# Kernel tuning notes

Measured on AMD Instinct MI355X. Metric: run time of the kernel, lower is better.

Reference implementation:

```python
import jax, jax.numpy as jnp
import numpy as np

B, S, E, H = 4, 2048, 1024, 16
HD = E // H  # head_dim = 64


def setup_inputs() -> dict:
    key = jax.random.key(0)
    k1, k2, k3, k4 = jax.random.split(key, 4)
    x = jax.random.normal(k1, (B, S, E), dtype=jnp.float32)
    # torch Linear stores weight as (out, in); y = x @ W.T
    w_qkv = jax.random.normal(k2, (3 * E, E), dtype=jnp.float32) * (E ** -0.5)
    w_proj = jax.random.normal(k3, (E, E), dtype=jnp.float32) * (E ** -0.5)
    b_proj = jax.random.normal(k4, (E,), dtype=jnp.float32) * 0.01
    return {"x": x, "w_qkv": w_qkv, "w_proj": w_proj, "b_proj": b_proj}


def reference(x, w_qkv, w_proj, b_proj):
    b, s, e = x.shape
    # fused QKV, then per-head interleaved split (matches view(B,S,H,3*hd).chunk)
    qkv = jnp.einsum('bse,fe->bsf', x, w_qkv).reshape(b, s, H, 3 * HD)
    q, k, v = jnp.split(qkv, 3, axis=-1)  # each (b, s, H, HD)
    scale = HD ** -0.5
    scores = jnp.einsum('bqhd,bkhd->bhqk', q, k) * scale
    causal = jnp.tril(jnp.ones((s, s), dtype=bool))
    scores = jnp.where(causal, scores, jnp.float32(-jnp.inf))
    probs = jax.nn.softmax(scores, axis=-1)
    out = jnp.einsum('bhqk,bkhd->bqhd', probs, v).reshape(b, s, e)
    return jnp.einsum('bse,fe->bsf', out, w_proj) + b_proj
```

## Files before the change

kernel.cpp:

```cpp
#include <hip/hip_runtime.h>

#define Bq   4
#define Sq   2048
#define Eq   1024
#define Hq   16
#define HDq  64
#define Mq   (Bq*Sq)
#define N1q  (3*Eq)
#define Kq   Eq

#define NX4  (Mq*Kq/4)
#define NW4  (N1q*Kq/4)
#define NP4  (Eq*Kq/4)

typedef __bf16 bf16x8 __attribute__((ext_vector_type(8)));
typedef __bf16 bf16x4 __attribute__((ext_vector_type(4)));
typedef float  f32x4  __attribute__((ext_vector_type(4)));
typedef float  f32x16 __attribute__((ext_vector_type(16)));

#define GAS __attribute__((address_space(1)))
#define LAS __attribute__((address_space(3)))

__device__ __forceinline__ void gl2lds16(const void* g, void* l) {
  __builtin_amdgcn_global_load_lds((GAS const void*)g, (LAS void*)l, 16, 0, 0);
}

__device__ __forceinline__ unsigned pack2(float a, float b) {
  union { __bf16 h[2]; unsigned u; } x;
  x.h[0] = (__bf16)a; x.h[1] = (__bf16)b; return x.u;
}

__device__ __forceinline__ void perm32swap(unsigned& a, unsigned& b) {
  asm("v_permlane32_swap_b32 %0, %1" : "+v"(a), "+v"(b));
}

__device__ __forceinline__ float fexp2(float x) {
#if __has_builtin(__builtin_amdgcn_exp2f)
  return __builtin_amdgcn_exp2f(x);
#else
  return exp2f(x);
#endif
}

__global__ __launch_bounds__(256) void cvt_all(const float* __restrict__ x,
                                               const float* __restrict__ wqkv,
                                               const float* __restrict__ wproj,
                                               __bf16* __restrict__ xb,
                                               __bf16* __restrict__ wqkvb,
                                               __bf16* __restrict__ wprojb) {
  int i = blockIdx.x * 256 + threadIdx.x;
  const float* src; __bf16* dst; int j; float sc = 1.0f;
  if (i < NX4) {
    src = x; dst = xb; j = i;
  } else if (i < NX4 + NW4) {
    j = i - NX4; src = wqkv; dst = wqkvb;
    const int row = j >> 8;
    if ((row % 192) < 64) sc = 0.18033688011112042f;
  } else {
    j = i - NX4 - NW4; src = wproj; dst = wprojb;
  }
  float4 v = ((const float4*)src)[j];
  bf16x4 o = { (__bf16)(v.x * sc), (__bf16)(v.y * sc),
               (__bf16)(v.z * sc), (__bf16)(v.w * sc) };
  ((bf16x4*)dst)[j] = o;
}

template <int MODE>
__global__ __launch_bounds__(256) void gemm_bt(const __bf16* __restrict__ A,
                                               const __bf16* __restrict__ Bw,
                                               int N, int K,
                                               __bf16* __restrict__ cbf,
                                               const float* __restrict__ bias,
                                               float* __restrict__ cf32) {
  __shared__ __align__(16) __bf16 As[128 * 64];
  __shared__ __align__(16) __bf16 Bs[128 * 64];
  const int tid  = threadIdx.x;
  const int wave = tid >> 6, lane = tid & 63;
  const int quad = lane >> 4, l15 = lane & 15;
  const int wm = wave & 1, wn = wave >> 1;
  const int bm0 = blockIdx.x * 128;
  const int bn0 = blockIdx.y * 128;

  f32x4 acc[4][4] = {};

  const int ar = tid >> 2;
  const int ac = ((tid & 3) ^ ((tid >> 3) & 3)) * 8;
  const __bf16* Ag0 = A  + (long)(bm0 + ar) * K + ac;
  const __bf16* Bg0 = Bw + (long)(bn0 + ar) * K + ac;
  __bf16* As0 = As + wave * 512;
  __bf16* Bs0 = Bs + wave * 512;

  const int fsw = (l15 >> 1) & 3;
  const int a_rd = (wm * 64 + l15) * 32 + (quad ^ fsw) * 8;
  const int b_rd = (wn * 64 + l15) * 32 + (quad ^ fsw) * 8;

  for (int kc = 0; kc < K; kc += 64) {
    gl2lds16(Ag0 + kc,               As0);
    gl2lds16(Ag0 + 64 * K + kc,      As0 + 2048);
    gl2lds16(Ag0 + kc + 32,          As0 + 4096);
    gl2lds16(Ag0 + 64 * K + kc + 32, As0 + 6144);
    gl2lds16(Bg0 + kc,               Bs0);
    gl2lds16(Bg0 + 64 * K + kc,      Bs0 + 2048);
    gl2lds16(Bg0 + kc + 32,          Bs0 + 4096);
    gl2lds16(Bg0 + 64 * K + kc + 32, Bs0 + 6144);
    __syncthreads();

    bf16x8 af[4], bfr[4];
#pragma unroll
    for (int mt = 0; mt < 4; mt++)
      af[mt] = *(const bf16x8*)&As[a_rd + mt * 512];
#pragma unroll
    for (int nt = 0; nt < 4; nt++)
      bfr[nt] = *(const bf16x8*)&Bs[b_rd + nt * 512];
#pragma unroll
    for (int mt = 0; mt < 4; mt++)
#pragma unroll
      for (int nt = 0; nt < 4; nt++)
        acc[mt][nt] = __builtin_amdgcn_mfma_f32_16x16x32_bf16(af[mt], bfr[nt], acc[mt][nt], 0, 0, 0);

    bf16x8 af1[4], bfr1[4];
#pragma unroll
    for (int mt = 0; mt < 4; mt++)
      af1[mt] = *(const bf16x8*)&As[4096 + a_rd + mt * 512];
#pragma unroll
    for (int nt = 0; nt < 4; nt++)
      bfr1[nt] = *(const bf16x8*)&Bs[4096 + b_rd + nt * 512];
#pragma unroll
    for (int mt = 0; mt < 4; mt++)
#pragma unroll
      for (int nt = 0; nt < 4; nt++)
        acc[mt][nt] = __builtin_amdgcn_mfma_f32_16x16x32_bf16(af1[mt], bfr1[nt], acc[mt][nt], 0, 0, 0);
    __syncthreads();
  }

#pragma unroll
  for (int nt = 0; nt < 4; nt++) {
    const int n = bn0 + wn * 64 + nt * 16 + l15;
    float bv = 0.f;
    if (MODE == 1) bv = bias[n];
#pragma unroll
    for (int mt = 0; mt < 4; mt++) {
      const int mbase = bm0 + wm * 64 + mt * 16 + quad * 4;
#pragma unroll
      for (int r = 0; r < 4; r++) {
        const long m = mbase + r;
        if (MODE == 0) cbf[m * N + n] = (__bf16)acc[mt][nt][r];
        else           cf32[m * N + n] = acc[mt][nt][r] + bv;
      }
    }
  }
}

__global__ __launch_bounds__(256) void transv(const __bf16* __restrict__ qkv,
                                              __bf16* __restrict__ vt) {
  __shared__ __align__(16) __bf16 T[64 * 64];
  const int tid = threadIdx.x, wave = tid >> 6;
  const int bh = blockIdx.x >> 5, st = blockIdx.x & 31;
  const int b = bh >> 4, h = bh & 15;
  const long gbase = (long)(b * Sq + st * 64 + (tid >> 3)) * N1q + h * 192 + 128 + (tid & 7) * 8;
  gl2lds16(qkv + gbase,                  T + wave * 512);
  gl2lds16(qkv + gbase + (long)32 * N1q, T + 2048 + wave * 512);
  __syncthreads();
  const int d = tid >> 2, s4 = (tid & 3) * 16;
  bf16x8 o0, o1;
#pragma unroll
  for (int j = 0; j < 8; j++) o0[j] = T[(s4 + j) * 64 + d];
#pragma unroll
  for (int j = 0; j < 8; j++) o1[j] = T[(s4 + 8 + j) * 64 + d];
  __bf16* dst = vt + (long)(bh * 64 + d) * Sq + st * 64 + s4;
  *(bf16x8*)dst = o0;
  *(bf16x8*)(dst + 8) = o1;
}

__global__ __launch_bounds__(256, 2) void attn_fwd(const __bf16* __restrict__ qkv,
                                                   const __bf16* __restrict__ vt,
                                                   __bf16* __restrict__ aout) {
  __shared__ __align__(16) __bf16 Ks0[128 * 64];
  __shared__ __align__(16) __bf16 Ks1[128 * 64];
  __shared__ __align__(16) __bf16 Vs0[64 * 128];
  __shared__ __align__(16) __bf16 Vs1[64 * 128];

  const int tid = threadIdx.x;
  const int w = tid >> 6, lane = tid & 63;
  const int c = lane & 31, h = lane >> 5;
  const int bi = blockIdx.x;
  const int bh = bi & 63, kk = (bi >> 6) & 3, jr = bi >> 8;
  const int qt = 4 * jr + ((kk + jr) & 3);
  const int b = bh >> 4, head = bh & 15;

  const int krr = lane >> 3, kj = lane & 7;
  const int vrr = lane >> 4, vj = lane & 15;

  const int q_g = qt * 128 + w * 32 + c;

  bf16x8 qf[4];
  const __bf16* qp = qkv + (long)(b * Sq + q_g) * N1q + head * 192 + h * 8;
#pragma unroll
  for (int kc2 = 0; kc2 < 4; kc2++) qf[kc2] = *(const bf16x8*)(qp + kc2 * 16);

  f32x16 oT[2] = {};
  float l_i = 0.f;
  constexpr float MB = 16.0f;

#define ATTN_STAGE(KD, VD, kt_) do {                                          \
    _Pragma("unroll")                                                         \
    for (int i = 0; i < 4; i++) {                                             \
      const int row = w * 32 + i * 8 + krr;                                   \
      gl2lds16(qkv + (long)(b * Sq + (kt_) * 128 + row) * N1q + head * 192    \
                   + 64 + (kj ^ (krr & 7)) * 8,                               \
               (KD) + (w * 32 + i * 8) * 64);                                 \
    }                                                                         \
    _Pragma("unroll")                                                         \
    for (int i = 0; i < 4; i++) {                                             \
      const int dr = w * 16 + i * 4 + vrr;                                    \
      gl2lds16(vt + (long)(bh * 64 + dr) * Sq + (kt_) * 128                   \
                  + (vj ^ (dr & 7)) * 8,                                      \
               (VD) + (w * 16 + i * 4) * 128);                                \
    }                                                                         \
  } while (0)

#define ATTN_COMPUTE(KS, VS, kt_) do {                                        \
    const bool diag = ((kt_) == qt);                                          \
    float s_acc = 0.f;                                                        \
    _Pragma("unroll")                                                         \
    for (int nf = 0; nf < 4; nf++) {                                          \
      f32x16 z;                                                               \
      _Pragma("unroll")                                                       \
      for (int r = 0; r < 16; r++) z[r] = -MB;    \
      _Pragma("unroll")                                                       \
      for (int kc2 = 0; kc2 < 4; kc2++) {                                     \
        bf16x8 kf = *(const bf16x8*)&(KS)[(nf * 32 + c) * 64                  \
                                          + (((kc2 * 2 + h) ^ (c & 7)) * 8)]; \
        z = __builtin_amdgcn_mfma_f32_32x32x16_bf16(kf, qf[kc2], z, 0, 0, 0); \
      }                                                                       \
      if (diag) {                                                             \
        _Pragma("unroll")                                                     \
        for (int r = 0; r < 16; r++) {                                        \
          const int kcol = (kt_) * 128 + nf * 32 + (r & 3) + 8 * (r >> 2)     \
                           + 4 * h;                                           \
          if (kcol > q_g) z[r] = -1e30f;                                      \
        }                                                                     \
      }                                                                       \
      _Pragma("unroll")                                                       \
      for (int r = 0; r < 16; r++) {                                          \
        float p = fexp2(z[r]);                                                \
        z[r] = p; s_acc += p;                                                 \
      }                                                                       \
      _Pragma("unroll")                                                       \
      for (int sub = 0; sub < 2; sub++) {                                     \
        const int kc = nf * 2 + sub, base = 8 * sub;                          \
        unsigned pa0 = pack2(z[base + 0], z[base + 1]);                       \
        unsigned pa1 = pack2(z[base + 2], z[base + 3]);                       \
        unsigned pb0 = pack2(z[base + 4], z[base + 5]);                       \
        unsigned pb1 = pack2(z[base + 6], z[base + 7]);                       \
        perm32swap(pa0, pb0);                                                 \
        perm32swap(pa1, pb1);                                                 \
        union { bf16x8 v; unsigned u[4]; } pf;                                \
        pf.u[0] = pa0; pf.u[1] = pa1; pf.u[2] = pb0; pf.u[3] = pb1;           \
        _Pragma("unroll")                                                     \
        for (int nf2 = 0; nf2 < 2; nf2++) {                                   \
          bf16x8 vf = *(const bf16x8*)&(VS)[(nf2 * 32 + c) * 128              \
                                            + (((kc * 2 + h) ^ (c & 7)) * 8)];\
          oT[nf2] = __builtin_amdgcn_mfma_f32_32x32x16_bf16(vf, pf.v,         \
                                                            oT[nf2], 0, 0, 0);\
        }                                                                     \
      }                                                                       \
    }                                                                         \
    l_i += s_acc;                                                             \
  } while (0)

  const int nk = qt + 1;
  ATTN_STAGE(Ks0, Vs0, 0);
  __syncthreads();

  int kt = 0;
  for (; kt + 1 < nk; kt += 2) {
    ATTN_STAGE(Ks1, Vs1, kt + 1);
    __builtin_amdgcn_sched_barrier(0);
    ATTN_COMPUTE(Ks0, Vs0, kt);
    __syncthreads();

    if (kt + 2 < nk) ATTN_STAGE(Ks0, Vs0, kt + 2);
    __builtin_amdgcn_sched_barrier(0);
    ATTN_COMPUTE(Ks1, Vs1, kt + 1);
    __syncthreads();
  }
  if (kt < nk)
    ATTN_COMPUTE(Ks0, Vs0, kt);

#undef ATTN_STAGE
#undef ATTN_COMPUTE

  const float l = l_i + __shfl_xor(l_i, 32);
  const float inv = 1.0f / l;
  const long obase = (long)(b * Sq + q_g) * Eq + head * 64;
#pragma unroll
  for (int nf2 = 0; nf2 < 2; nf2++)
#pragma unroll
    for (int g = 0; g < 4; g++) {
      bf16x4 o;
#pragma unroll
      for (int t = 0; t < 4; t++) o[t] = (__bf16)(oT[nf2][g * 4 + t] * inv);
      *(bf16x4*)(aout + obase + nf2 * 32 + 8 * g + 4 * h) = o;
    }
}

extern "C" void kernel_launch(void* const* d_in, const int* in_sizes, int n_in,
                              void* d_out, int out_size, void* d_ws, size_t ws_size,
                              hipStream_t stream) {
  const float* x      = (const float*)d_in[0];
  const float* w_qkv  = (const float*)d_in[1];
  const float* w_proj = (const float*)d_in[2];
  const float* b_proj = (const float*)d_in[3];
  float* out = (float*)d_out;

  char* w = (char*)d_ws;
  __bf16* xb     = (__bf16*)w; w += (size_t)Mq * Kq * 2;
  __bf16* wqkvb  = (__bf16*)w; w += (size_t)N1q * Kq * 2;
  __bf16* wprojb = (__bf16*)w; w += (size_t)Eq * Kq * 2;
  __bf16* qkvb   = (__bf16*)w; w += (size_t)Mq * N1q * 2;
  __bf16* vtb    = (__bf16*)w; w += (size_t)Bq * Hq * HDq * Sq * 2;
  __bf16* attnb  = (__bf16*)w;

  cvt_all<<<(NX4 + NW4 + NP4) / 256, 256, 0, stream>>>(x, w_qkv, w_proj, xb, wqkvb, wprojb);

  gemm_bt<0><<<dim3(Mq / 128, N1q / 128), 256, 0, stream>>>(xb, wqkvb, N1q, Kq, qkvb, nullptr, nullptr);

  transv<<<Bq * Hq * (Sq / 64), 256, 0, stream>>>(qkvb, vtb);

  attn_fwd<<<16 * 64, 256, 0, stream>>>(qkvb, vtb, attnb);

  gemm_bt<1><<<dim3(Mq / 128, Eq / 128), 256, 0, stream>>>(attnb, wprojb, Eq, Kq, nullptr, b_proj, out);
}
```

Measured before the change: 252.3 us.

## Replace double-buffered LDS DMA with register-staged K/V prefetch in attention

The attention kernel drops its double-buffered K/V LDS tiles and the direct global-to-LDS loads. It now loads the next K/V tile into registers during compute and writes it to a single LDS buffer between two barriers. This halves LDS use (possibly raising occupancy) and overlaps global latency with a full tile of compute. In exchange it adds register pressure, an extra barrier per tile and explicit LDS write instructions.

```diff
diff --git a/kernel.cpp b/kernel.cpp
--- a/kernel.cpp
+++ b/kernel.cpp
@@ -175,10 +175,8 @@
 __global__ __launch_bounds__(256, 2) void attn_fwd(const __bf16* __restrict__ qkv,
                                                    const __bf16* __restrict__ vt,
                                                    __bf16* __restrict__ aout) {
-  __shared__ __align__(16) __bf16 Ks0[128 * 64];
-  __shared__ __align__(16) __bf16 Ks1[128 * 64];
-  __shared__ __align__(16) __bf16 Vs0[64 * 128];
-  __shared__ __align__(16) __bf16 Vs1[64 * 128];
+  __shared__ __align__(16) __bf16 Ks[128 * 64];
+  __shared__ __align__(16) __bf16 Vs[64 * 128];
 
   const int tid = threadIdx.x;
   const int w = tid >> 6, lane = tid & 63;
@@ -202,24 +200,40 @@
   float l_i = 0.f;
   constexpr float MB = 16.0f;
 
-#define ATTN_STAGE(KD, VD, kt_) do {                                          \
-    _Pragma("unroll")                                                         \
-    for (int i = 0; i < 4; i++) {                                             \
-      const int row = w * 32 + i * 8 + krr;                                   \
-      gl2lds16(qkv + (long)(b * Sq + (kt_) * 128 + row) * N1q + head * 192    \
-                   + 64 + (kj ^ (krr & 7)) * 8,                               \
-               (KD) + (w * 32 + i * 8) * 64);                                 \
-    }                                                                         \
-    _Pragma("unroll")                                                         \
-    for (int i = 0; i < 4; i++) {                                             \
-      const int dr = w * 16 + i * 4 + vrr;                                    \
-      gl2lds16(vt + (long)(bh * 64 + dr) * Sq + (kt_) * 128                   \
-                  + (vj ^ (dr & 7)) * 8,                                      \
-               (VD) + (w * 16 + i * 4) * 128);                                \
-    }                                                                         \
+  uint4 rk0, rk1, rk2, rk3, rv0, rv1, rv2, rv3;
+  const char* gK = (const char*)qkv +
+      2 * ((long)(b * Sq + w * 32 + krr) * N1q + head * 192 + 64 + (kj ^ (krr & 7)) * 8);
+  const char* gV = (const char*)vt + 2 * ((long)(bh * 64 + w * 16 + vrr) * Sq);
+  const int o0 = (vj ^ vrr) * 16, o1 = o0 ^ 64;
+  __bf16* ldsK = Ks + w * 2048 + lane * 8;
+  __bf16* ldsV = Vs + w * 2048 + lane * 8;
+
+#define LOADKV(kt_) do {                                                      \
+    const char* kp_ = gK + (long)(kt_) * (128L * N1q * 2);                    \
+    rk0 = *(const uint4*)(kp_);                                               \
+    rk1 = *(const uint4*)(kp_ + 1L * 8 * N1q * 2);                            \
+    rk2 = *(const uint4*)(kp_ + 2L * 8 * N1q * 2);                            \
+    rk3 = *(const uint4*)(kp_ + 3L * 8 * N1q * 2);                            \
+    const char* vp_ = gV + (long)(kt_) * 256;                                 \
+    rv0 = *(const uint4*)(vp_ + 0 * 16384 + o0);                              \
+    rv1 = *(const uint4*)(vp_ + 1 * 16384 + o1);                              \
+    rv2 = *(const uint4*)(vp_ + 2 * 16384 + o0);                              \
+    rv3 = *(const uint4*)(vp_ + 3 * 16384 + o1);                              \
   } while (0)
 
-#define ATTN_COMPUTE(KS, VS, kt_) do {                                        \
+#define WRITEKV() do {                                                        \
+    union { uint4 u; bf16x8 b; } t_;                                          \
+    t_.u = rk0; *(bf16x8*)(ldsK +    0) = t_.b;                               \
+    t_.u = rk1; *(bf16x8*)(ldsK +  512) = t_.b;                               \
+    t_.u = rk2; *(bf16x8*)(ldsK + 1024) = t_.b;                               \
+    t_.u = rk3; *(bf16x8*)(ldsK + 1536) = t_.b;                               \
+    t_.u = rv0; *(bf16x8*)(ldsV +    0) = t_.b;                               \
+    t_.u = rv1; *(bf16x8*)(ldsV +  512) = t_.b;                               \
+    t_.u = rv2; *(bf16x8*)(ldsV + 1024) = t_.b;                               \
+    t_.u = rv3; *(bf16x8*)(ldsV + 1536) = t_.b;                               \
+  } while (0)
+
+#define ATTN_COMPUTE(kt_) do {                                                \
     const bool diag = ((kt_) == qt);                                          \
     float s_acc = 0.f;                                                        \
     _Pragma("unroll")                                                         \
@@ -229,8 +243,8 @@
       for (int r = 0; r < 16; r++) z[r] = -MB;    \
       _Pragma("unroll")                                                       \
       for (int kc2 = 0; kc2 < 4; kc2++) {                                     \
-        bf16x8 kf = *(const bf16x8*)&(KS)[(nf * 32 + c) * 64                  \
-                                          + (((kc2 * 2 + h) ^ (c & 7)) * 8)]; \
+        bf16x8 kf = *(const bf16x8*)&Ks[(nf * 32 + c) * 64                    \
+                                        + (((kc2 * 2 + h) ^ (c & 7)) * 8)];   \
         z = __builtin_amdgcn_mfma_f32_32x32x16_bf16(kf, qf[kc2], z, 0, 0, 0); \
       }                                                                       \
       if (diag) {                                                             \
@@ -259,8 +273,8 @@
         pf.u[0] = pa0; pf.u[1] = pa1; pf.u[2] = pb0; pf.u[3] = pb1;           \
         _Pragma("unroll")                                                     \
         for (int nf2 = 0; nf2 < 2; nf2++) {                                   \
-          bf16x8 vf = *(const bf16x8*)&(VS)[(nf2 * 32 + c) * 128              \
-                                            + (((kc * 2 + h) ^ (c & 7)) * 8)];\
+          bf16x8 vf = *(const bf16x8*)&Vs[(nf2 * 32 + c) * 128                \
+                                          + (((kc * 2 + h) ^ (c & 7)) * 8)];  \
           oT[nf2] = __builtin_amdgcn_mfma_f32_32x32x16_bf16(vf, pf.v,         \
                                                             oT[nf2], 0, 0, 0);\
         }                                                                     \
@@ -270,25 +284,23 @@
   } while (0)
 
   const int nk = qt + 1;
-  ATTN_STAGE(Ks0, Vs0, 0);
+
+  LOADKV(0);
+  WRITEKV();
   __syncthreads();
-
-  int kt = 0;
-  for (; kt + 1 < nk; kt += 2) {
-    ATTN_STAGE(Ks1, Vs1, kt + 1);
+  if (nk > 1) LOADKV(1);
+
+  for (int kt = 0; kt < nk; kt++) {
     __builtin_amdgcn_sched_barrier(0);
-    ATTN_COMPUTE(Ks0, Vs0, kt);
+    ATTN_COMPUTE(kt);
     __syncthreads();
-
-    if (kt + 2 < nk) ATTN_STAGE(Ks0, Vs0, kt + 2);
-    __builtin_amdgcn_sched_barrier(0);
-    ATTN_COMPUTE(Ks1, Vs1, kt + 1);
+    if (kt + 1 < nk) WRITEKV();
     __syncthreads();
+    if (kt + 2 < nk) LOADKV(kt + 2);
   }
-  if (kt < nk)
-    ATTN_COMPUTE(Ks0, Vs0, kt);
-
-#undef ATTN_STAGE
+
+#undef LOADKV
+#undef WRITEKV
 #undef ATTN_COMPUTE
 
   const float l = l_i + __shfl_xor(l_i, 32);
```

Result: faster. 241.4 us (-4.3%).
